# Kernel tuning notes

Measured on AMD Instinct MI355X. Metric: run time of the kernel, lower is better.

## Reference

```python
import jax, jax.numpy as jnp
import numpy as np

# ---- problem constants (from init_kwargs) ----
B, NJ = 65536, 32
TARGET_LINKS = (8, 16, 24, 32)
POS_W, ORI_W, POSE_W = 1.0, 0.5, 1.0
LIMIT_W, REST_W = 10.0, 0.1
BASE_POS_W, BASE_ORI_W = 5.0, 5.0

# ---- SE3 math (pose = [t(3), quat xyzw(4)]) ----

def quat_mul(q1, q2):
    v1, w1 = q1[..., :3], q1[..., 3:4]
    v2, w2 = q2[..., :3], q2[..., 3:4]
    w = w1 * w2 - jnp.sum(v1 * v2, -1, keepdims=True)
    v = w1 * v2 + w2 * v1 + jnp.cross(v1, v2)
    return jnp.concatenate([v, w], -1)

def quat_rotate(q, t):
    v, w = q[..., :3], q[..., 3:4]
    return t + 2.0 * jnp.cross(v, jnp.cross(v, t) + w * t)

def se3_compose(T1, T2):
    t1, q1 = T1[..., :3], T1[..., 3:]
    t2, q2 = T2[..., :3], T2[..., 3:]
    return jnp.concatenate([t1 + quat_rotate(q1, t2), quat_mul(q1, q2)], -1)

def se3_inverse(T):
    t, q = T[..., :3], T[..., 3:]
    qinv = jnp.concatenate([-q[..., :3], q[..., 3:4]], -1)
    return jnp.concatenate([-quat_rotate(qinv, t), qinv], -1)

def quat_log(q):
    # canonicalize to w >= 0 (shortest rotation)
    q = jnp.where(q[..., 3:4] < 0.0, -q, q)
    v, w = q[..., :3], q[..., 3:4]
    nv2 = jnp.sum(v * v, -1, keepdims=True)
    nv = jnp.sqrt(jnp.maximum(nv2, 1e-14))
    angle = 2.0 * jnp.arctan2(nv, w)
    small = nv < 1e-6
    w_safe = jnp.where(jnp.abs(w) > 1e-8, w, 1.0)
    scale = jnp.where(small, 2.0 / w_safe, angle / nv)
    return v * scale  # phi, |phi| = rotation angle

def se3_log(T):
    # returns 6-vector [rho(3), phi(3)]
    t, q = T[..., :3], T[..., 3:]
    phi = quat_log(q)
    th2 = jnp.sum(phi * phi, -1, keepdims=True)
    th = jnp.sqrt(jnp.maximum(th2, 1e-14))
    small = th < 1e-4
    ths = jnp.where(small, 1.0, th)  # safe theta for non-small branch
    a = jnp.where(small,
                  1.0 / 12.0 + th2 / 720.0,
                  (1.0 - ths * jnp.sin(ths) / (2.0 * (1.0 - jnp.cos(ths)))) / (ths * ths))
    # rho = V^{-1}(phi) @ t, with hat(phi) x = cross(phi, x)
    pt = jnp.cross(phi, t)
    rho = t - 0.5 * pt + a * jnp.cross(phi, pt)
    return jnp.concatenate([rho, phi], -1)

def forward_kinematics(cfg, base, joint_offsets, joint_axes):
    # cfg [B, NJ], base [B,7] -> fk [B, NJ+1, 7]
    def step(T, inp):
        off, ax, th = inp  # [7], [3], [B]
        T = se3_compose(T, off[None, :])
        half = 0.5 * th[:, None]
        jq = jnp.concatenate([ax[None, :] * jnp.sin(half), jnp.cos(half)], -1)  # [B,4]
        # compose with pure-rotation joint transform (zero translation)
        T = jnp.concatenate([T[..., :3], quat_mul(T[..., 3:], jq)], -1)
        return T, T
    _, poses = jax.lax.scan(step, base, (joint_offsets, joint_axes, cfg.T))  # [NJ,B,7]
    return jnp.concatenate([base[:, None, :], jnp.swapaxes(poses, 0, 1)], 1)

# ---- inputs ----

def _rand_pose(key, shape):
    k1, k2 = jax.random.split(key)
    t = jax.random.normal(k1, shape + (3,), dtype=jnp.float32) * 0.5
    q = jax.random.normal(k2, shape + (4,), dtype=jnp.float32)
    q = q / jnp.linalg.norm(q, axis=-1, keepdims=True)
    return jnp.concatenate([t, q], -1)

def setup_inputs() -> dict:
    key = jax.random.key(0)
    ks = jax.random.split(key, 9)
    cfg = jax.random.normal(ks[0], (B, NJ), dtype=jnp.float32) * 0.3
    default_base = _rand_pose(ks[1], ())
    base = _rand_pose(ks[2], (B,))
    target_poses = _rand_pose(ks[3], (len(TARGET_LINKS),))
    joint_offsets = _rand_pose(ks[4], (NJ,))
    ax = jax.random.normal(ks[5], (NJ, 3), dtype=jnp.float32)
    joint_axes = ax / jnp.linalg.norm(ax, axis=-1, keepdims=True)
    rest_cfg = jax.random.normal(ks[6], (NJ,), dtype=jnp.float32) * 0.2
    joint_lower = -jnp.abs(jax.random.normal(ks[7], (NJ,), dtype=jnp.float32)) - 1.0
    joint_upper = jnp.abs(jax.random.normal(ks[8], (NJ,), dtype=jnp.float32)) + 1.0
    return dict(cfg=cfg, base=base, target_poses=target_poses, default_base=default_base,
                rest_cfg=rest_cfg, joint_offsets=joint_offsets, joint_axes=joint_axes,
                joint_lower=joint_lower, joint_upper=joint_upper)

# ---- forward ----

def reference(cfg, base, target_poses, default_base, rest_cfg,
              joint_offsets, joint_axes, joint_lower, joint_upper):
    fk = forward_kinematics(cfg, base, joint_offsets, joint_axes)  # [B, NJ+1, 7]
    actual = fk[:, jnp.array(TARGET_LINKS), :]                     # [B, T, 7]
    T_err = se3_compose(se3_inverse(target_poses)[None, :, :], actual)
    log_err = se3_log(T_err)                                       # [B, T, 6]
    w6 = jnp.concatenate([jnp.full((3,), POS_W, jnp.float32),
                          jnp.full((3,), ORI_W, jnp.float32)]) * POSE_W
    pose_res = (log_err * w6).reshape(cfg.shape[0], -1)            # [B, 6T]
    limit_res = (jnp.maximum(cfg - joint_upper, 0.0) + jnp.minimum(cfg - joint_lower, 0.0)) * LIMIT_W
    rest_res = (cfg - rest_cfg) * REST_W
    base_err = se3_log(se3_compose(se3_inverse(default_base)[None, :], base))  # [B,6]
    base_res = jnp.concatenate([base_err[:, :3] * BASE_POS_W, base_err[:, 3:] * BASE_ORI_W], -1)
    return jnp.concatenate([pose_res, limit_res, rest_res, base_res], -1)  # [B, 6T+2NJ+6]
```

## Files before the change

kernel.cpp:

```cpp
#include <hip/hip_runtime.h>

#define NB 65536
#define NJ 32
#define BLK 128

struct V3 { float x, y, z; };
struct Q4 { float x, y, z, w; };

__device__ __forceinline__ V3 v3cross(V3 a, V3 b) {
    V3 r;
    r.x = a.y * b.z - a.z * b.y;
    r.y = a.z * b.x - a.x * b.z;
    r.z = a.x * b.y - a.y * b.x;
    return r;
}

__device__ __forceinline__ Q4 qmul(Q4 a, Q4 b) {
    Q4 r;
    r.x = a.w * b.x + b.w * a.x + (a.y * b.z - a.z * b.y);
    r.y = a.w * b.y + b.w * a.y + (a.z * b.x - a.x * b.z);
    r.z = a.w * b.z + b.w * a.z + (a.x * b.y - a.y * b.x);
    r.w = a.w * b.w - (a.x * b.x + a.y * b.y + a.z * b.z);
    return r;
}

__device__ __forceinline__ V3 qrot(Q4 q, V3 t) {
    V3 v = {q.x, q.y, q.z};
    V3 u = v3cross(v, t);
    u.x += q.w * t.x; u.y += q.w * t.y; u.z += q.w * t.z;
    V3 c = v3cross(v, u);
    V3 r = {t.x + 2.f * c.x, t.y + 2.f * c.y, t.z + 2.f * c.z};
    return r;
}

__device__ __forceinline__ V3 quat_log(Q4 q) {
    float s = (q.w < 0.f) ? -1.f : 1.f;
    float x = q.x * s, y = q.y * s, z = q.z * s, w = q.w * s;
    float nv2 = x * x + y * y + z * z;
    float nv = sqrtf(fmaxf(nv2, 1e-14f));
    float angle = 2.f * atan2f(nv, w);
    float w_safe = (fabsf(w) > 1e-8f) ? w : 1.f;
    float scale = (nv < 1e-6f) ? (2.f / w_safe) : (angle / nv);
    V3 r = {x * scale, y * scale, z * scale};
    return r;
}

__device__ __forceinline__ void se3_log(V3 t, Q4 q, float* o6) {
    V3 phi = quat_log(q);
    float th2 = phi.x * phi.x + phi.y * phi.y + phi.z * phi.z;
    float th = sqrtf(fmaxf(th2, 1e-14f));
    bool small = th < 1e-4f;
    float ths = small ? 1.f : th;
    float sn = sinf(ths), cs = cosf(ths);
    float a_big = (1.f - ths * sn / (2.f * (1.f - cs))) / (ths * ths);
    float a = small ? (1.f / 12.f + th2 / 720.f) : a_big;
    V3 pt = v3cross(phi, t);
    V3 ppt = v3cross(phi, pt);
    o6[0] = t.x - 0.5f * pt.x + a * ppt.x;
    o6[1] = t.y - 0.5f * pt.y + a * ppt.y;
    o6[2] = t.z - 0.5f * pt.z + a * ppt.z;
    o6[3] = phi.x;
    o6[4] = phi.y;
    o6[5] = phi.z;
}

__global__ __launch_bounds__(BLK) void ik_kernel(
    const float* __restrict__ cfg,
    const float* __restrict__ base,
    const float* __restrict__ tposes,
    const float* __restrict__ dbase,
    const float* __restrict__ restc,
    const float* __restrict__ joff,
    const float* __restrict__ jaxes,
    const float* __restrict__ jlo,
    const float* __restrict__ jup,
    float* __restrict__ out)
{
    __shared__ float s_offt[NJ][3];
    __shared__ float s_offq[NJ][4];
    __shared__ float s_ax[NJ][3];
    __shared__ float s_lo[NJ];
    __shared__ float s_up[NJ];
    __shared__ float s_rest[NJ];
    __shared__ float s_ti[4][7];
    __shared__ float s_dbi[7];
    __shared__ __align__(16) float s_out[BLK * 94];

    const int tid = threadIdx.x;

    if (tid < NJ) {
        const int j = tid;
        s_offt[j][0] = joff[j * 7 + 0];
        s_offt[j][1] = joff[j * 7 + 1];
        s_offt[j][2] = joff[j * 7 + 2];
        s_offq[j][0] = joff[j * 7 + 3];
        s_offq[j][1] = joff[j * 7 + 4];
        s_offq[j][2] = joff[j * 7 + 5];
        s_offq[j][3] = joff[j * 7 + 6];
        s_ax[j][0] = jaxes[j * 3 + 0];
        s_ax[j][1] = jaxes[j * 3 + 1];
        s_ax[j][2] = jaxes[j * 3 + 2];
        s_lo[j] = jlo[j];
        s_up[j] = jup[j];
        s_rest[j] = restc[j];
    } else if (tid < 36) {
        const int i = tid - 32;
        V3 t = {tposes[i * 7 + 0], tposes[i * 7 + 1], tposes[i * 7 + 2]};
        Q4 q = {tposes[i * 7 + 3], tposes[i * 7 + 4], tposes[i * 7 + 5], tposes[i * 7 + 6]};
        Q4 qi = {-q.x, -q.y, -q.z, q.w};
        V3 rt = qrot(qi, t);
        s_ti[i][0] = -rt.x; s_ti[i][1] = -rt.y; s_ti[i][2] = -rt.z;
        s_ti[i][3] = qi.x;  s_ti[i][4] = qi.y;  s_ti[i][5] = qi.z;  s_ti[i][6] = qi.w;
    } else if (tid == 36) {
        V3 t = {dbase[0], dbase[1], dbase[2]};
        Q4 q = {dbase[3], dbase[4], dbase[5], dbase[6]};
        Q4 qi = {-q.x, -q.y, -q.z, q.w};
        V3 rt = qrot(qi, t);
        s_dbi[0] = -rt.x; s_dbi[1] = -rt.y; s_dbi[2] = -rt.z;
        s_dbi[3] = qi.x;  s_dbi[4] = qi.y;  s_dbi[5] = qi.z;  s_dbi[6] = qi.w;
    }
    __syncthreads();

    const int b = blockIdx.x * BLK + tid;

    float cf[NJ];
    {
        const float4* cp = reinterpret_cast<const float4*>(cfg + (size_t)b * NJ);
        #pragma unroll
        for (int v = 0; v < 8; ++v) {
            float4 d = cp[v];
            cf[v * 4 + 0] = d.x;
            cf[v * 4 + 1] = d.y;
            cf[v * 4 + 2] = d.z;
            cf[v * 4 + 3] = d.w;
        }
    }

    const float* bp = base + (size_t)b * 7;
    V3 b_t = {bp[0], bp[1], bp[2]};
    Q4 b_q = {bp[3], bp[4], bp[5], bp[6]};

    float* o = s_out + tid * 94;

    V3 Tt = b_t;
    Q4 Tq = b_q;
    #pragma unroll
    for (int j = 0; j < NJ; ++j) {
        V3 ot = {s_offt[j][0], s_offt[j][1], s_offt[j][2]};
        Q4 oq = {s_offq[j][0], s_offq[j][1], s_offq[j][2], s_offq[j][3]};
        V3 rt = qrot(Tq, ot);
        Tt.x += rt.x; Tt.y += rt.y; Tt.z += rt.z;
        Tq = qmul(Tq, oq);
        float half = 0.5f * cf[j];
        float sh, ch;
        sincosf(half, &sh, &ch);
        Q4 jq = {s_ax[j][0] * sh, s_ax[j][1] * sh, s_ax[j][2] * sh, ch};
        Tq = qmul(Tq, jq);

        if ((j & 7) == 7) {
            const int i = j >> 3;
            V3 it = {s_ti[i][0], s_ti[i][1], s_ti[i][2]};
            Q4 iq = {s_ti[i][3], s_ti[i][4], s_ti[i][5], s_ti[i][6]};
            V3 et = qrot(iq, Tt);
            et.x += it.x; et.y += it.y; et.z += it.z;
            Q4 eq = qmul(iq, Tq);
            float l6[6];
            se3_log(et, eq, l6);
            o[i * 6 + 0] = l6[0];
            o[i * 6 + 1] = l6[1];
            o[i * 6 + 2] = l6[2];
            o[i * 6 + 3] = l6[3] * 0.5f;
            o[i * 6 + 4] = l6[4] * 0.5f;
            o[i * 6 + 5] = l6[5] * 0.5f;
        }
    }

    #pragma unroll
    for (int j = 0; j < NJ; ++j) {
        float c = cf[j];
        float lim = (fmaxf(c - s_up[j], 0.f) + fminf(c - s_lo[j], 0.f)) * 10.f;
        o[24 + j] = lim;
        o[56 + j] = (c - s_rest[j]) * 0.1f;
    }

    {
        V3 it = {s_dbi[0], s_dbi[1], s_dbi[2]};
        Q4 iq = {s_dbi[3], s_dbi[4], s_dbi[5], s_dbi[6]};
        V3 et = qrot(iq, b_t);
        et.x += it.x; et.y += it.y; et.z += it.z;
        Q4 eq = qmul(iq, b_q);
        float l6[6];
        se3_log(et, eq, l6);
        o[88] = l6[0] * 5.f;
        o[89] = l6[1] * 5.f;
        o[90] = l6[2] * 5.f;
        o[91] = l6[3] * 5.f;
        o[92] = l6[4] * 5.f;
        o[93] = l6[5] * 5.f;
    }

    __syncthreads();

    {
        const uint4* src = reinterpret_cast<const uint4*>(s_out);
        uint4* dst = reinterpret_cast<uint4*>(out + (size_t)blockIdx.x * BLK * 94);
        #pragma unroll
        for (int i = 0; i < 24; ++i) {
            int idx = i * BLK + tid;
            if (idx < 3008) dst[idx] = src[idx];
        }
    }
}

extern "C" void kernel_launch(void* const* d_in, const int* in_sizes, int n_in,
                              void* d_out, int out_size, void* d_ws, size_t ws_size,
                              hipStream_t stream) {
    const float* cfg   = (const float*)d_in[0];
    const float* base  = (const float*)d_in[1];
    const float* tp    = (const float*)d_in[2];
    const float* db    = (const float*)d_in[3];
    const float* rest  = (const float*)d_in[4];
    const float* joff  = (const float*)d_in[5];
    const float* jax   = (const float*)d_in[6];
    const float* jlo   = (const float*)d_in[7];
    const float* jup   = (const float*)d_in[8];
    float* out = (float*)d_out;

    ik_kernel<<<NB / BLK, BLK, 0, stream>>>(cfg, base, tp, db, rest, joff, jax, jlo, jup, out);
}
```

Before: 100.8 us.

## Split FK chain across 4 lanes per row with shuffle prefix-scan of SE3 transforms

Each batch row is now handled by four threads, each composing an 8-joint segment of the kinematic chain. The segments are combined with a two-step warp-shuffle inclusive scan over SE3 composition, then each lane applies the base pose and computes one target's log error. Base poses are staged through shared memory with coalesced float2 loads, and sin/cos use fast intrinsics. The aim is to shorten the serial per-thread dependency chain, cut register pressure and raise parallelism, at the cost of shuffle traffic, redundant composition work and lower-precision trig.

```diff
diff --git a/kernel.cpp b/kernel.cpp
--- a/kernel.cpp
+++ b/kernel.cpp
@@ -1,8 +1,9 @@
 #include <hip/hip_runtime.h>
 
+#define NJ 32
+#define ROWS_PER_BLK 64
+#define BLK 256
 #define NB 65536
-#define NJ 32
-#define BLK 128
 
 struct V3 { float x, y, z; };
 struct Q4 { float x, y, z, w; };
@@ -51,7 +52,7 @@
     float th = sqrtf(fmaxf(th2, 1e-14f));
     bool small = th < 1e-4f;
     float ths = small ? 1.f : th;
-    float sn = sinf(ths), cs = cosf(ths);
+    float sn = __sinf(ths), cs = __cosf(ths);
     float a_big = (1.f - ths * sn / (2.f * (1.f - cs))) / (ths * ths);
     float a = small ? (1.f / 12.f + th2 / 720.f) : a_big;
     V3 pt = v3cross(phi, t);
@@ -76,27 +77,28 @@
     const float* __restrict__ jup,
     float* __restrict__ out)
 {
-    __shared__ float s_offt[NJ][3];
-    __shared__ float s_offq[NJ][4];
+    __shared__ float s_mt[NJ][3];
+    __shared__ float s_oq[NJ][4];
     __shared__ float s_ax[NJ][3];
     __shared__ float s_lo[NJ];
     __shared__ float s_up[NJ];
     __shared__ float s_rest[NJ];
     __shared__ float s_ti[4][7];
     __shared__ float s_dbi[7];
-    __shared__ __align__(16) float s_out[BLK * 94];
+    __shared__ __align__(8)  float s_base[ROWS_PER_BLK * 7];
+    __shared__ __align__(16) float s_out[ROWS_PER_BLK * 94];
 
     const int tid = threadIdx.x;
 
     if (tid < NJ) {
         const int j = tid;
-        s_offt[j][0] = joff[j * 7 + 0];
-        s_offt[j][1] = joff[j * 7 + 1];
-        s_offt[j][2] = joff[j * 7 + 2];
-        s_offq[j][0] = joff[j * 7 + 3];
-        s_offq[j][1] = joff[j * 7 + 4];
-        s_offq[j][2] = joff[j * 7 + 5];
-        s_offq[j][3] = joff[j * 7 + 6];
+        s_mt[j][0] = joff[j * 7 + 0];
+        s_mt[j][1] = joff[j * 7 + 1];
+        s_mt[j][2] = joff[j * 7 + 2];
+        s_oq[j][0] = joff[j * 7 + 3];
+        s_oq[j][1] = joff[j * 7 + 4];
+        s_oq[j][2] = joff[j * 7 + 5];
+        s_oq[j][3] = joff[j * 7 + 6];
         s_ax[j][0] = jaxes[j * 3 + 0];
         s_ax[j][1] = jaxes[j * 3 + 1];
         s_ax[j][2] = jaxes[j * 3 + 2];
@@ -119,71 +121,101 @@
         s_dbi[0] = -rt.x; s_dbi[1] = -rt.y; s_dbi[2] = -rt.z;
         s_dbi[3] = qi.x;  s_dbi[4] = qi.y;  s_dbi[5] = qi.z;  s_dbi[6] = qi.w;
     }
+    if (tid < 224) {
+        reinterpret_cast<float2*>(s_base)[tid] =
+            reinterpret_cast<const float2*>(base + (size_t)blockIdx.x * ROWS_PER_BLK * 7)[tid];
+    }
     __syncthreads();
 
-    const int b = blockIdx.x * BLK + tid;
-
-    float cf[NJ];
-    {
-        const float4* cp = reinterpret_cast<const float4*>(cfg + (size_t)b * NJ);
-        #pragma unroll
-        for (int v = 0; v < 8; ++v) {
-            float4 d = cp[v];
-            cf[v * 4 + 0] = d.x;
-            cf[v * 4 + 1] = d.y;
-            cf[v * 4 + 2] = d.z;
-            cf[v * 4 + 3] = d.w;
-        }
-    }
-
-    const float* bp = base + (size_t)b * 7;
-    V3 b_t = {bp[0], bp[1], bp[2]};
-    Q4 b_q = {bp[3], bp[4], bp[5], bp[6]};
-
-    float* o = s_out + tid * 94;
-
-    V3 Tt = b_t;
-    Q4 Tq = b_q;
+    const int r   = tid >> 2;
+    const int sub = tid & 3;
+    const size_t b = (size_t)blockIdx.x * ROWS_PER_BLK + r;
+    const int j0 = sub * 8;
+
+    float cf[8];
+    {
+        const float4* cp = reinterpret_cast<const float4*>(cfg + b * NJ + j0);
+        float4 c0 = cp[0], c1 = cp[1];
+        cf[0] = c0.x; cf[1] = c0.y; cf[2] = c0.z; cf[3] = c0.w;
+        cf[4] = c1.x; cf[5] = c1.y; cf[6] = c1.z; cf[7] = c1.w;
+    }
+
+    V3 St; Q4 Sq;
+    {
+        float half = 0.5f * cf[0];
+        float sh = __sinf(half), ch = __cosf(half);
+        Q4 jq = {s_ax[j0][0] * sh, s_ax[j0][1] * sh, s_ax[j0][2] * sh, ch};
+        Q4 oq = {s_oq[j0][0], s_oq[j0][1], s_oq[j0][2], s_oq[j0][3]};
+        Sq = qmul(oq, jq);
+        St.x = s_mt[j0][0]; St.y = s_mt[j0][1]; St.z = s_mt[j0][2];
+    }
     #pragma unroll
-    for (int j = 0; j < NJ; ++j) {
-        V3 ot = {s_offt[j][0], s_offt[j][1], s_offt[j][2]};
-        Q4 oq = {s_offq[j][0], s_offq[j][1], s_offq[j][2], s_offq[j][3]};
-        V3 rt = qrot(Tq, ot);
-        Tt.x += rt.x; Tt.y += rt.y; Tt.z += rt.z;
-        Tq = qmul(Tq, oq);
-        float half = 0.5f * cf[j];
-        float sh, ch;
-        sincosf(half, &sh, &ch);
+    for (int k = 1; k < 8; ++k) {
+        const int j = j0 + k;
+        float half = 0.5f * cf[k];
+        float sh = __sinf(half), ch = __cosf(half);
         Q4 jq = {s_ax[j][0] * sh, s_ax[j][1] * sh, s_ax[j][2] * sh, ch};
-        Tq = qmul(Tq, jq);
-
-        if ((j & 7) == 7) {
-            const int i = j >> 3;
-            V3 it = {s_ti[i][0], s_ti[i][1], s_ti[i][2]};
-            Q4 iq = {s_ti[i][3], s_ti[i][4], s_ti[i][5], s_ti[i][6]};
-            V3 et = qrot(iq, Tt);
-            et.x += it.x; et.y += it.y; et.z += it.z;
-            Q4 eq = qmul(iq, Tq);
-            float l6[6];
-            se3_log(et, eq, l6);
-            o[i * 6 + 0] = l6[0];
-            o[i * 6 + 1] = l6[1];
-            o[i * 6 + 2] = l6[2];
-            o[i * 6 + 3] = l6[3] * 0.5f;
-            o[i * 6 + 4] = l6[4] * 0.5f;
-            o[i * 6 + 5] = l6[5] * 0.5f;
-        }
+        Q4 oq = {s_oq[j][0], s_oq[j][1], s_oq[j][2], s_oq[j][3]};
+        Q4 mq = qmul(oq, jq);
+        V3 mt = {s_mt[j][0], s_mt[j][1], s_mt[j][2]};
+        V3 rt = qrot(Sq, mt);
+        St.x += rt.x; St.y += rt.y; St.z += rt.z;
+        Sq = qmul(Sq, mq);
     }
 
     #pragma unroll
-    for (int j = 0; j < NJ; ++j) {
-        float c = cf[j];
+    for (int d = 1; d <= 2; d <<= 1) {
+        V3 Ut; Q4 Uq;
+        Ut.x = __shfl_up(St.x, d, 4);
+        Ut.y = __shfl_up(St.y, d, 4);
+        Ut.z = __shfl_up(St.z, d, 4);
+        Uq.x = __shfl_up(Sq.x, d, 4);
+        Uq.y = __shfl_up(Sq.y, d, 4);
+        Uq.z = __shfl_up(Sq.z, d, 4);
+        Uq.w = __shfl_up(Sq.w, d, 4);
+        V3 ct = qrot(Uq, St);
+        ct.x += Ut.x; ct.y += Ut.y; ct.z += Ut.z;
+        Q4 cq = qmul(Uq, Sq);
+        bool take = (sub >= d);
+        St.x = take ? ct.x : St.x; St.y = take ? ct.y : St.y; St.z = take ? ct.z : St.z;
+        Sq.x = take ? cq.x : Sq.x; Sq.y = take ? cq.y : Sq.y;
+        Sq.z = take ? cq.z : Sq.z; Sq.w = take ? cq.w : Sq.w;
+    }
+
+    V3 b_t = {s_base[r * 7 + 0], s_base[r * 7 + 1], s_base[r * 7 + 2]};
+    Q4 b_q = {s_base[r * 7 + 3], s_base[r * 7 + 4], s_base[r * 7 + 5], s_base[r * 7 + 6]};
+    V3 Tt = qrot(b_q, St);
+    Tt.x += b_t.x; Tt.y += b_t.y; Tt.z += b_t.z;
+    Q4 Tq = qmul(b_q, Sq);
+
+    float* o = s_out + r * 94;
+
+    {
+        V3 it = {s_ti[sub][0], s_ti[sub][1], s_ti[sub][2]};
+        Q4 iq = {s_ti[sub][3], s_ti[sub][4], s_ti[sub][5], s_ti[sub][6]};
+        V3 et = qrot(iq, Tt);
+        et.x += it.x; et.y += it.y; et.z += it.z;
+        Q4 eq = qmul(iq, Tq);
+        float l6[6];
+        se3_log(et, eq, l6);
+        o[sub * 6 + 0] = l6[0];
+        o[sub * 6 + 1] = l6[1];
+        o[sub * 6 + 2] = l6[2];
+        o[sub * 6 + 3] = l6[3] * 0.5f;
+        o[sub * 6 + 4] = l6[4] * 0.5f;
+        o[sub * 6 + 5] = l6[5] * 0.5f;
+    }
+
+    #pragma unroll
+    for (int k = 0; k < 8; ++k) {
+        const int j = j0 + k;
+        float c = cf[k];
         float lim = (fmaxf(c - s_up[j], 0.f) + fminf(c - s_lo[j], 0.f)) * 10.f;
         o[24 + j] = lim;
         o[56 + j] = (c - s_rest[j]) * 0.1f;
     }
 
-    {
+    if (sub == 0) {
         V3 it = {s_dbi[0], s_dbi[1], s_dbi[2]};
         Q4 iq = {s_dbi[3], s_dbi[4], s_dbi[5], s_dbi[6]};
         V3 et = qrot(iq, b_t);
@@ -203,11 +235,11 @@
 
     {
         const uint4* src = reinterpret_cast<const uint4*>(s_out);
-        uint4* dst = reinterpret_cast<uint4*>(out + (size_t)blockIdx.x * BLK * 94);
+        uint4* dst = reinterpret_cast<uint4*>(out + (size_t)blockIdx.x * ROWS_PER_BLK * 94);
         #pragma unroll
-        for (int i = 0; i < 24; ++i) {
+        for (int i = 0; i < 6; ++i) {
             int idx = i * BLK + tid;
-            if (idx < 3008) dst[idx] = src[idx];
+            if (idx < 1504) dst[idx] = src[idx];
         }
     }
 }
@@ -226,5 +258,5 @@
     const float* jup   = (const float*)d_in[8];
     float* out = (float*)d_out;
 
-    ik_kernel<<<NB / BLK, BLK, 0, stream>>>(cfg, base, tp, db, rest, joff, jax, jlo, jup, out);
-}
+    ik_kernel<<<NB / ROWS_PER_BLK, BLK, 0, stream>>>(cfg, base, tp, db, rest, joff, jax, jlo, jup, out);
+}
```

After: 91.93 us (median of 2 runs). 1.1x faster.
